# Performance work log

Measured on AMD Instinct MI355X. Metric: run time of the kernel, lower is better.

## Reference

```python
import jax, jax.numpy as jnp
import numpy as np


def setup_inputs() -> dict:
    key = jax.random.key(0)
    k1, k2, k3, k4 = jax.random.split(key, 4)
    B, T, C, H = 4, 2048, 1024, 64
    x = jax.random.normal(k1, (B, T, C), dtype=jnp.float32)
    # nn.Linear(n_embd, head_size, bias=False) weights, stored as [in, out]
    s = 1.0 / np.sqrt(C)
    Wk = jax.random.normal(k2, (C, H), dtype=jnp.float32) * s
    Wq = jax.random.normal(k3, (C, H), dtype=jnp.float32) * s
    Wv = jax.random.normal(k4, (C, H), dtype=jnp.float32) * s
    return {"x": x, "Wk": Wk, "Wq": Wq, "Wv": Wv}


def reference(x, Wk, Wq, Wv):
    B, T, C = x.shape
    k = x @ Wk  # [B,T,H]
    q = x @ Wq  # [B,T,H]
    v = x @ Wv  # [B,T,H]
    # NOTE: original scales by C**-0.5 where C = n_embd (faithful quirk).
    scale = jnp.asarray(C, x.dtype) ** -0.5
    wei = jnp.einsum('bth,bsh->bts', q, k) * scale  # [B,T,T]
    causal = jnp.tril(jnp.ones((T, T), dtype=bool))
    wei = jnp.where(causal, wei, -jnp.inf)
    wei = jax.nn.softmax(wei, axis=-1)
    # dropout is identity in eval mode / for deterministic reference
    return jnp.einsum('bts,bsh->bth', wei, v)
```

## Files before the change

kernel.cpp:

```cpp
#include <hip/hip_runtime.h>

#define B_ 4
#define T_ 2048
#define C_ 1024
#define H_ 64
#define M_ (B_*T_)

typedef __bf16 bf16x8 __attribute__((ext_vector_type(8)));
typedef float f32x4 __attribute__((ext_vector_type(4)));
typedef short short8 __attribute__((ext_vector_type(8)));
typedef float float4v __attribute__((ext_vector_type(4)));

static __device__ __forceinline__ f32x4 mfma16(bf16x8 a, bf16x8 b, f32x4 c) {
    return __builtin_amdgcn_mfma_f32_16x16x32_bf16(a, b, c, 0, 0, 0);
}
static __device__ __forceinline__ unsigned short f2bfu(float f) {
    return __builtin_bit_cast(unsigned short, (__bf16)f);
}

__global__ __launch_bounds__(256) void wconv_kernel(const float* __restrict__ Wk,
                                                    const float* __restrict__ Wq,
                                                    const float* __restrict__ Wv,
                                                    unsigned short* __restrict__ Wtf) {
    int t = blockIdx.x * 256 + threadIdx.x;
    int f = t >> 6;
    int l = t & 63;
    int n = f % 12, kk = f / 12;
    int sel = n >> 2;
    int wcol = (n & 3) * 16 + (l & 15);
    int kbase = kk * 32 + (l >> 4) * 8;
    const float* W = (sel == 0) ? Wk : ((sel == 1) ? Wq : Wv);
    float scale = (sel == 1) ? 0.03125f : 1.0f;
    unsigned short* dst = Wtf + f * 512 + l * 8;
#pragma unroll
    for (int j = 0; j < 8; ++j)
        dst[j] = f2bfu(W[(kbase + j) * 64 + wcol] * scale);
}

__global__ __launch_bounds__(256) void proj_kernel(const float* __restrict__ x,
                                                   const unsigned short* __restrict__ Wtf,
                                                   unsigned short* __restrict__ kbuf,
                                                   unsigned short* __restrict__ qbuf,
                                                   unsigned short* __restrict__ vbuf) {
    int tid = threadIdx.x;
    int l = tid & 63, lm = l & 15, lg = l >> 4;
    int w = tid >> 6;
    int r0 = blockIdx.x * 16;

    f32x4 acc[3];
#pragma unroll
    for (int nn = 0; nn < 3; ++nn) acc[nn] = f32x4{0.f, 0.f, 0.f, 0.f};

    const float* xp = x + (r0 + lm) * C_ + lg * 8;
    const unsigned short* wp = Wtf + (w * 3) * 512 + l * 8;

    float4v a0 = *(const float4v*)(xp);
    float4v a1 = *(const float4v*)(xp + 4);
    short8 b0 = *(const short8*)(wp);
    short8 b1 = *(const short8*)(wp + 512);
    short8 b2 = *(const short8*)(wp + 1024);

    for (int kk = 0; kk < 31; ++kk) {
        xp += 32; wp += 12 * 512;
        float4v na0 = *(const float4v*)(xp);
        float4v na1 = *(const float4v*)(xp + 4);
        short8 nb0 = *(const short8*)(wp);
        short8 nb1 = *(const short8*)(wp + 512);
        short8 nb2 = *(const short8*)(wp + 1024);
        bf16x8 af;
#pragma unroll
        for (int j = 0; j < 4; ++j) { af[j] = (__bf16)a0[j]; af[4 + j] = (__bf16)a1[j]; }
        acc[0] = mfma16(af, __builtin_bit_cast(bf16x8, b0), acc[0]);
        acc[1] = mfma16(af, __builtin_bit_cast(bf16x8, b1), acc[1]);
        acc[2] = mfma16(af, __builtin_bit_cast(bf16x8, b2), acc[2]);
        a0 = na0; a1 = na1; b0 = nb0; b1 = nb1; b2 = nb2;
    }
    {
        bf16x8 af;
#pragma unroll
        for (int j = 0; j < 4; ++j) { af[j] = (__bf16)a0[j]; af[4 + j] = (__bf16)a1[j]; }
        acc[0] = mfma16(af, __builtin_bit_cast(bf16x8, b0), acc[0]);
        acc[1] = mfma16(af, __builtin_bit_cast(bf16x8, b1), acc[1]);
        acc[2] = mfma16(af, __builtin_bit_cast(bf16x8, b2), acc[2]);
    }

    int tg0 = r0 + lg * 4;
#pragma unroll
    for (int nn = 0; nn < 3; ++nn) {
        int n = w * 3 + nn;
        int sel = n >> 2;
        int col = (n & 3) * 16 + lm;
        unsigned short* dst = (sel == 0) ? kbuf : ((sel == 1) ? qbuf : vbuf);
#pragma unroll
        for (int i = 0; i < 4; ++i)
            dst[(tg0 + i) * H_ + col] = f2bfu(acc[nn][i]);
    }
}

__global__ __launch_bounds__(256) void kvconv_kernel(unsigned short* __restrict__ kbuf,
                                                     unsigned short* __restrict__ vbuf) {
    __shared__ alignas(16) unsigned short klds[32][72];
    __shared__ alignas(16) unsigned short vlds[32][72];
    int tid = threadIdx.x;
    int bj = blockIdx.x;
    unsigned short* kt = kbuf + bj * 2048;
    unsigned short* vt = vbuf + bj * 2048;

    int row = tid >> 3, cq = (tid & 7) * 8;
    short8 kv = *(const short8*)(kt + row * 64 + cq);
    short8 vv = *(const short8*)(vt + row * 64 + cq);
    *(short8*)(&klds[row][cq]) = kv;
    *(short8*)(&vlds[row][cq]) = vv;
    __syncthreads();

    int l = tid & 63, lm = l & 15, lg = l >> 4;
    int f = tid >> 6;
    int kk = f >> 1, nn = f & 1;
    short8 kf = *(const short8*)(&klds[nn * 16 + lm][kk * 32 + lg * 8]);
    short8 vf;
#pragma unroll
    for (int jj = 0; jj < 8; ++jj)
        vf[jj] = (short)vlds[lg * 8 + jj][f * 16 + lm];

    *(short8*)(kt + f * 512 + l * 8) = kf;
    *(short8*)(vt + f * 512 + l * 8) = vf;
}

__global__ __launch_bounds__(256) void attn_kernel(const unsigned short* __restrict__ kbuf,
                                                   const unsigned short* __restrict__ qbuf,
                                                   const unsigned short* __restrict__ vbuf,
                                                   float* __restrict__ out) {
    int tid = threadIdx.x;
    int l = tid & 63, lm = l & 15, lg = l >> 4;
    int w = tid >> 6;
    int bid = blockIdx.x;
    int xcd = bid & 7, ii = bid >> 3;
    int b = xcd >> 1;
    int qtl = ii * 2 + (xcd & 1);
    int q0 = (127 - qtl) * 16;

    __shared__ alignas(16) unsigned short plds[4][16][72];
    __shared__ float olds[4][16][64];
    __shared__ float mlds[4][16];
    __shared__ float llds[4][16];

    bf16x8 qf[2];
#pragma unroll
    for (int kk = 0; kk < 2; ++kk)
        qf[kk] = __builtin_bit_cast(bf16x8,
            *(const short8*)(qbuf + (b * T_ + q0 + lm) * H_ + kk * 32 + lg * 8));

    f32x4 of[4];
#pragma unroll
    for (int nh = 0; nh < 4; ++nh) of[nh] = f32x4{0.f, 0.f, 0.f, 0.f};
    float mrun[4], lrun[4];
#pragma unroll
    for (int i = 0; i < 4; ++i) { mrun[i] = -1e30f; lrun[i] = 0.f; }

    int nj = q0 / 64 + 1;

    for (int J = w; J < nj; J += 4) {
        f32x4 s[4];
#pragma unroll
        for (int n = 0; n < 4; ++n) s[n] = f32x4{0.f, 0.f, 0.f, 0.f};
#pragma unroll
        for (int kk = 0; kk < 2; ++kk) {
#pragma unroll
            for (int n = 0; n < 4; ++n) {
                const unsigned short* kp = kbuf +
                    (((b * 64 + 2 * J + (n >> 1)) * 2 + kk) * 2 + (n & 1)) * 512 + l * 8;
                s[n] = mfma16(qf[kk], __builtin_bit_cast(bf16x8, *(const short8*)kp), s[n]);
            }
        }
        if (J == nj - 1) {
#pragma unroll
            for (int n = 0; n < 4; ++n) {
                int kc = J * 64 + n * 16 + lm;
#pragma unroll
                for (int i = 0; i < 4; ++i) {
                    int qr = q0 + lg * 4 + i;
                    if (kc > qr) s[n][i] = -1e30f;
                }
            }
        }
        float alpha[4];
#pragma unroll
        for (int i = 0; i < 4; ++i) {
            float pm = fmaxf(fmaxf(s[0][i], s[1][i]), fmaxf(s[2][i], s[3][i]));
#pragma unroll
            for (int d = 1; d < 16; d <<= 1) pm = fmaxf(pm, __shfl_xor(pm, d, 64));
            float mn = fmaxf(mrun[i], pm);
            float al = __expf(mrun[i] - mn);
            float rs = 0.f;
#pragma unroll
            for (int n = 0; n < 4; ++n) {
                float e = __expf(s[n][i] - mn);
                s[n][i] = e; rs += e;
            }
#pragma unroll
            for (int d = 1; d < 16; d <<= 1) rs += __shfl_xor(rs, d, 64);
            lrun[i] = lrun[i] * al + rs;
            mrun[i] = mn;
            alpha[i] = al;
        }
#pragma unroll
        for (int nh = 0; nh < 4; ++nh)
#pragma unroll
            for (int i = 0; i < 4; ++i) of[nh][i] *= alpha[i];

#pragma unroll
        for (int n = 0; n < 4; ++n)
#pragma unroll
            for (int i = 0; i < 4; ++i)
                plds[w][lg * 4 + i][n * 16 + lm] = f2bfu(s[n][i]);
        bf16x8 pf[2];
#pragma unroll
        for (int ks = 0; ks < 2; ++ks)
            pf[ks] = __builtin_bit_cast(bf16x8,
                *(const short8*)(&plds[w][lm][ks * 32 + lg * 8]));
#pragma unroll
        for (int nh = 0; nh < 4; ++nh) {
#pragma unroll
            for (int ks = 0; ks < 2; ++ks) {
                const unsigned short* vp = vbuf +
                    ((b * 64 + 2 * J + ks) * 4 + nh) * 512 + l * 8;
                of[nh] = mfma16(pf[ks], __builtin_bit_cast(bf16x8, *(const short8*)vp), of[nh]);
            }
        }
    }

#pragma unroll
    for (int nh = 0; nh < 4; ++nh)
#pragma unroll
        for (int i = 0; i < 4; ++i)
            olds[w][lg * 4 + i][nh * 16 + lm] = of[nh][i];
    if (lm == 0) {
#pragma unroll
        for (int i = 0; i < 4; ++i) {
            mlds[w][lg * 4 + i] = mrun[i];
            llds[w][lg * 4 + i] = lrun[i];
        }
    }
    __syncthreads();

#pragma unroll
    for (int i = 0; i < 4; ++i) {
        int row = lg * 4 + i;
        float m0 = mlds[0][row], m1 = mlds[1][row], m2 = mlds[2][row], m3 = mlds[3][row];
        float M = fmaxf(fmaxf(m0, m1), fmaxf(m2, m3));
        float e0 = __expf(m0 - M), e1 = __expf(m1 - M);
        float e2 = __expf(m2 - M), e3 = __expf(m3 - M);
        float L = llds[0][row] * e0 + llds[1][row] * e1 + llds[2][row] * e2 + llds[3][row] * e3;
        int cc = w * 16 + lm;
        float o = olds[0][row][cc] * e0 + olds[1][row][cc] * e1 +
                  olds[2][row][cc] * e2 + olds[3][row][cc] * e3;
        out[(b * T_ + q0 + row) * H_ + cc] = o / L;
    }
}

extern "C" void kernel_launch(void* const* d_in, const int* in_sizes, int n_in,
                              void* d_out, int out_size, void* d_ws, size_t ws_size,
                              hipStream_t stream) {
    const float* x  = (const float*)d_in[0];
    const float* Wk = (const float*)d_in[1];
    const float* Wq = (const float*)d_in[2];
    const float* Wv = (const float*)d_in[3];
    float* out = (float*)d_out;

    unsigned short* ws   = (unsigned short*)d_ws;
    unsigned short* Wtf  = ws;
    unsigned short* kbuf = Wtf + 384 * 512;
    unsigned short* qbuf = kbuf + M_ * H_;
    unsigned short* vbuf = qbuf + M_ * H_;

    wconv_kernel<<<dim3(96), dim3(256), 0, stream>>>(Wk, Wq, Wv, Wtf);
    proj_kernel<<<dim3(M_ / 16), dim3(256), 0, stream>>>(x, Wtf, kbuf, qbuf, vbuf);
    kvconv_kernel<<<dim3(B_ * 64), dim3(256), 0, stream>>>(kbuf, vbuf);
    attn_kernel<<<dim3(B_ * (T_ / 16)), dim3(256), 0, stream>>>(kbuf, qbuf, vbuf, out);
}
```

Measured before the change: 112.8 us.

## Transpose QK^T MFMA so softmax is per-lane and split KV over 8 waves

Swaps the MFMA operands so each lane holds one query row of the score tile. Row max and sum then reduce mostly in registers with two cross-lane shuffles instead of four butterfly stages per row. The attention block doubles to 512 threads, with 8 waves splitting the key blocks, and the final merge is rewritten to combine 8 partial results. This raises parallelism per query tile but adds LDS usage and a larger reduction, and it broadcasts alpha back through shuffles.

New measurement: 106.9 us. 1.05x faster.

```diff
diff --git a/kernel.cpp b/kernel.cpp
--- a/kernel.cpp
+++ b/kernel.cpp
@@ -9,6 +9,7 @@
 typedef __bf16 bf16x8 __attribute__((ext_vector_type(8)));
 typedef float f32x4 __attribute__((ext_vector_type(4)));
 typedef short short8 __attribute__((ext_vector_type(8)));
+typedef short short4v __attribute__((ext_vector_type(4)));
 typedef float float4v __attribute__((ext_vector_type(4)));
 
 static __device__ __forceinline__ f32x4 mfma16(bf16x8 a, bf16x8 b, f32x4 c) {
@@ -126,7 +127,7 @@
     *(short8*)(vt + f * 512 + l * 8) = vf;
 }
 
-__global__ __launch_bounds__(256) void attn_kernel(const unsigned short* __restrict__ kbuf,
+__global__ __launch_bounds__(512) void attn_kernel(const unsigned short* __restrict__ kbuf,
                                                    const unsigned short* __restrict__ qbuf,
                                                    const unsigned short* __restrict__ vbuf,
                                                    float* __restrict__ out) {
@@ -139,10 +140,10 @@
     int qtl = ii * 2 + (xcd & 1);
     int q0 = (127 - qtl) * 16;
 
-    __shared__ alignas(16) unsigned short plds[4][16][72];
-    __shared__ float olds[4][16][64];
-    __shared__ float mlds[4][16];
-    __shared__ float llds[4][16];
+    __shared__ alignas(16) unsigned short plds[8][16][72];
+    __shared__ float olds[8][16][64];
+    __shared__ float mlds[8][16];
+    __shared__ float llds[8][16];
 
     bf16x8 qf[2];
 #pragma unroll
@@ -153,13 +154,11 @@
     f32x4 of[4];
 #pragma unroll
     for (int nh = 0; nh < 4; ++nh) of[nh] = f32x4{0.f, 0.f, 0.f, 0.f};
-    float mrun[4], lrun[4];
-#pragma unroll
-    for (int i = 0; i < 4; ++i) { mrun[i] = -1e30f; lrun[i] = 0.f; }
+    float mrun = -1e30f, lrun = 0.f;
 
     int nj = q0 / 64 + 1;
 
-    for (int J = w; J < nj; J += 4) {
+    for (int J = w; J < nj; J += 8) {
         f32x4 s[4];
 #pragma unroll
         for (int n = 0; n < 4; ++n) s[n] = f32x4{0.f, 0.f, 0.f, 0.f};
@@ -169,50 +168,56 @@
             for (int n = 0; n < 4; ++n) {
                 const unsigned short* kp = kbuf +
                     (((b * 64 + 2 * J + (n >> 1)) * 2 + kk) * 2 + (n & 1)) * 512 + l * 8;
-                s[n] = mfma16(qf[kk], __builtin_bit_cast(bf16x8, *(const short8*)kp), s[n]);
+                s[n] = mfma16(__builtin_bit_cast(bf16x8, *(const short8*)kp), qf[kk], s[n]);
             }
         }
         if (J == nj - 1) {
+            int qr = q0 + lm;
 #pragma unroll
             for (int n = 0; n < 4; ++n) {
-                int kc = J * 64 + n * 16 + lm;
-#pragma unroll
-                for (int i = 0; i < 4; ++i) {
-                    int qr = q0 + lg * 4 + i;
-                    if (kc > qr) s[n][i] = -1e30f;
-                }
+                int kc0 = J * 64 + (n >> 1) * 32 + (n & 1) * 16 + lg * 4;
+#pragma unroll
+                for (int i = 0; i < 4; ++i)
+                    if (kc0 + i > qr) s[n][i] = -1e30f;
             }
         }
-        float alpha[4];
-#pragma unroll
-        for (int i = 0; i < 4; ++i) {
-            float pm = fmaxf(fmaxf(s[0][i], s[1][i]), fmaxf(s[2][i], s[3][i]));
-#pragma unroll
-            for (int d = 1; d < 16; d <<= 1) pm = fmaxf(pm, __shfl_xor(pm, d, 64));
-            float mn = fmaxf(mrun[i], pm);
-            float al = __expf(mrun[i] - mn);
-            float rs = 0.f;
-#pragma unroll
-            for (int n = 0; n < 4; ++n) {
-                float e = __expf(s[n][i] - mn);
-                s[n][i] = e; rs += e;
-            }
-#pragma unroll
-            for (int d = 1; d < 16; d <<= 1) rs += __shfl_xor(rs, d, 64);
-            lrun[i] = lrun[i] * al + rs;
-            mrun[i] = mn;
-            alpha[i] = al;
-        }
+        float pm0 = fmaxf(fmaxf(s[0][0], s[0][1]), fmaxf(s[0][2], s[0][3]));
+        float pm1 = fmaxf(fmaxf(s[1][0], s[1][1]), fmaxf(s[1][2], s[1][3]));
+        float pm2 = fmaxf(fmaxf(s[2][0], s[2][1]), fmaxf(s[2][2], s[2][3]));
+        float pm3 = fmaxf(fmaxf(s[3][0], s[3][1]), fmaxf(s[3][2], s[3][3]));
+        float pm = fmaxf(fmaxf(pm0, pm1), fmaxf(pm2, pm3));
+        pm = fmaxf(pm, __shfl_xor(pm, 16, 64));
+        pm = fmaxf(pm, __shfl_xor(pm, 32, 64));
+        float mn = fmaxf(mrun, pm);
+        float al = __expf(mrun - mn);
+        float rsn[4];
+#pragma unroll
+        for (int n = 0; n < 4; ++n) {
+            float e0 = __expf(s[n][0] - mn), e1 = __expf(s[n][1] - mn);
+            float e2 = __expf(s[n][2] - mn), e3 = __expf(s[n][3] - mn);
+            s[n][0] = e0; s[n][1] = e1; s[n][2] = e2; s[n][3] = e3;
+            rsn[n] = (e0 + e1) + (e2 + e3);
+        }
+        float rs = (rsn[0] + rsn[1]) + (rsn[2] + rsn[3]);
+        rs += __shfl_xor(rs, 16, 64);
+        rs += __shfl_xor(rs, 32, 64);
+        lrun = lrun * al + rs;
+        mrun = mn;
+        float alv[4];
+#pragma unroll
+        for (int i = 0; i < 4; ++i) alv[i] = __shfl(al, lg * 4 + i, 64);
 #pragma unroll
         for (int nh = 0; nh < 4; ++nh)
 #pragma unroll
-            for (int i = 0; i < 4; ++i) of[nh][i] *= alpha[i];
-
-#pragma unroll
-        for (int n = 0; n < 4; ++n)
-#pragma unroll
-            for (int i = 0; i < 4; ++i)
-                plds[w][lg * 4 + i][n * 16 + lm] = f2bfu(s[n][i]);
+            for (int i = 0; i < 4; ++i) of[nh][i] *= alv[i];
+
+#pragma unroll
+        for (int n = 0; n < 4; ++n) {
+            short4v pv;
+#pragma unroll
+            for (int i = 0; i < 4; ++i) pv[i] = (short)f2bfu(s[n][i]);
+            *(short4v*)(&plds[w][lm][(n >> 1) * 32 + (n & 1) * 16 + lg * 4]) = pv;
+        }
         bf16x8 pf[2];
 #pragma unroll
         for (int ks = 0; ks < 2; ++ks)
@@ -234,27 +239,31 @@
 #pragma unroll
         for (int i = 0; i < 4; ++i)
             olds[w][lg * 4 + i][nh * 16 + lm] = of[nh][i];
-    if (lm == 0) {
-#pragma unroll
-        for (int i = 0; i < 4; ++i) {
-            mlds[w][lg * 4 + i] = mrun[i];
-            llds[w][lg * 4 + i] = lrun[i];
-        }
+    if (l < 16) {
+        mlds[w][l] = mrun;
+        llds[w][l] = lrun;
     }
     __syncthreads();
 
-#pragma unroll
-    for (int i = 0; i < 4; ++i) {
-        int row = lg * 4 + i;
-        float m0 = mlds[0][row], m1 = mlds[1][row], m2 = mlds[2][row], m3 = mlds[3][row];
-        float M = fmaxf(fmaxf(m0, m1), fmaxf(m2, m3));
-        float e0 = __expf(m0 - M), e1 = __expf(m1 - M);
-        float e2 = __expf(m2 - M), e3 = __expf(m3 - M);
-        float L = llds[0][row] * e0 + llds[1][row] * e1 + llds[2][row] * e2 + llds[3][row] * e3;
-        int cc = w * 16 + lm;
-        float o = olds[0][row][cc] * e0 + olds[1][row][cc] * e1 +
-                  olds[2][row][cc] * e2 + olds[3][row][cc] * e3;
-        out[(b * T_ + q0 + row) * H_ + cc] = o / L;
+    int row = tid >> 5;
+    int c0 = tid & 31;
+    float mw[8];
+#pragma unroll
+    for (int u = 0; u < 8; ++u) mw[u] = mlds[u][row];
+    float M = fmaxf(fmaxf(fmaxf(mw[0], mw[1]), fmaxf(mw[2], mw[3])),
+                    fmaxf(fmaxf(mw[4], mw[5]), fmaxf(mw[6], mw[7])));
+    float ew[8];
+    float L = 0.f;
+#pragma unroll
+    for (int u = 0; u < 8; ++u) { ew[u] = __expf(mw[u] - M); L += llds[u][row] * ew[u]; }
+    float invL = 1.0f / L;
+#pragma unroll
+    for (int h = 0; h < 2; ++h) {
+        int col = c0 + h * 32;
+        float o = 0.f;
+#pragma unroll
+        for (int u = 0; u < 8; ++u) o += olds[u][row][col] * ew[u];
+        out[(b * T_ + q0 + row) * H_ + col] = o * invL;
     }
 }
 
@@ -276,5 +285,5 @@
     wconv_kernel<<<dim3(96), dim3(256), 0, stream>>>(Wk, Wq, Wv, Wtf);
     proj_kernel<<<dim3(M_ / 16), dim3(256), 0, stream>>>(x, Wtf, kbuf, qbuf, vbuf);
     kvconv_kernel<<<dim3(B_ * 64), dim3(256), 0, stream>>>(kbuf, vbuf);
-    attn_kernel<<<dim3(B_ * (T_ / 16)), dim3(256), 0, stream>>>(kbuf, qbuf, vbuf, out);
-}
+    attn_kernel<<<dim3(B_ * (T_ / 16)), dim3(512), 0, stream>>>(kbuf, qbuf, vbuf, out);
+}
```
